# Kernel tuning notes

Measured on AMD Instinct MI355X. Metric: run time of the kernel, lower is better.

Reference implementation:

```python
import jax, jax.numpy as jnp
import numpy as np

D_MODEL = 768
NUM_HEADS = 8
DEPTH = D_MODEL // NUM_HEADS


def setup_inputs() -> dict:
    key = jax.random.key(0)
    ks = jax.random.split(key, 12)
    B, S = 4, 2048
    s = 0.02
    return {
        "q_in": jax.random.normal(ks[0], (B, S, D_MODEL), jnp.float32),
        "k_in": jax.random.normal(ks[1], (B, S, D_MODEL), jnp.float32),
        "v_in": jax.random.normal(ks[2], (B, S, D_MODEL), jnp.float32),
        "mask": jnp.zeros((B, 1, 1, S), jnp.float32),
        "wq": jax.random.normal(ks[3], (D_MODEL, D_MODEL), jnp.float32) * s,
        "bq": jax.random.normal(ks[4], (D_MODEL,), jnp.float32) * s,
        "wk": jax.random.normal(ks[5], (D_MODEL, D_MODEL), jnp.float32) * s,
        "bk": jax.random.normal(ks[6], (D_MODEL,), jnp.float32) * s,
        "wv": jax.random.normal(ks[7], (D_MODEL, D_MODEL), jnp.float32) * s,
        "bv": jax.random.normal(ks[8], (D_MODEL,), jnp.float32) * s,
        "wo": jax.random.normal(ks[9], (D_MODEL, D_MODEL), jnp.float32) * s,
        "bo": jax.random.normal(ks[10], (D_MODEL,), jnp.float32) * s,
    }


def _split_heads(x, B):
    # [B, S, D] -> [B, H, S, depth]
    return x.reshape(B, -1, NUM_HEADS, DEPTH).transpose(0, 2, 1, 3)


def reference(q_in, k_in, v_in, mask, wq, bq, wk, bk, wv, bv, wo, bo):
    B = q_in.shape[0]
    q = _split_heads(q_in @ wq + bq, B)   # [B,H,Sq,d]
    k = _split_heads(k_in @ wk + bk, B)   # [B,H,Sk,d]
    v = _split_heads(v_in @ wv + bv, B)   # [B,H,Sk,d]

    scale = 1.0 / jnp.sqrt(jnp.float32(DEPTH))
    logits = jnp.einsum("bhqd,bhkd->bhqk", q, k) * scale
    logits = logits + mask * (-1e9)
    attn = jax.nn.softmax(logits, axis=-1)            # [B,H,Sq,Sk]
    ctx = jnp.einsum("bhqk,bhkd->bhqd", attn, v)
    ctx = ctx.transpose(0, 2, 1, 3).reshape(B, -1, D_MODEL)  # concat heads
    out = ctx @ wo + bo
    return out, attn
```

## Files before the change

kernel.cpp:

```cpp
#include <hip/hip_runtime.h>
#include <hip/hip_bf16.h>
#include <stdint.h>


#define SEQ 2048
#define DM 768
#define NB 4
#define NH 8
#define DEP 96
#define MROWS 8192

typedef __bf16 bf16x8 __attribute__((ext_vector_type(8)));
typedef float f32x4 __attribute__((ext_vector_type(4)));

__device__ inline unsigned short f2b(float f) {
    return __builtin_bit_cast(unsigned short, (__bf16)f);
}
__device__ inline bf16x8 ld_frag(const unsigned short* p) {
    return __builtin_bit_cast(bf16x8, *(const uint4*)p);
}

__global__ __launch_bounds__(256) void wt_kernel(
    const float* __restrict__ w0, const float* __restrict__ w1,
    const float* __restrict__ w2, const float* __restrict__ w3,
    unsigned short* __restrict__ wt)
{
    __shared__ float tile[32][33];
    int mat = blockIdx.z;
    const float* w = mat == 0 ? w0 : mat == 1 ? w1 : mat == 2 ? w2 : w3;
    unsigned short* dst = wt + (size_t)mat * DM * DM;
    int k0 = blockIdx.x * 32, n0 = blockIdx.y * 32;
    int tx = threadIdx.x & 31, ty = threadIdx.x >> 5;
#pragma unroll
    for (int i = 0; i < 4; i++)
        tile[ty + i * 8][tx] = w[(size_t)(k0 + ty + i * 8) * DM + n0 + tx];
    __syncthreads();
#pragma unroll
    for (int i = 0; i < 4; i++)
        dst[(size_t)(n0 + ty + i * 8) * DM + k0 + tx] = f2b(tile[tx][ty + i * 8]);
}

__global__ __launch_bounds__(256) void proj_kernel(
    const float* __restrict__ qin, const float* __restrict__ kin, const float* __restrict__ vin,
    const unsigned short* __restrict__ wt,
    const float* __restrict__ bq, const float* __restrict__ bk, const float* __restrict__ bv,
    unsigned short* __restrict__ qb, unsigned short* __restrict__ kb, unsigned short* __restrict__ vb)
{
    int z = blockIdx.z;
    const float* x = z == 0 ? qin : z == 1 ? kin : vin;
    const unsigned short* W = wt + (size_t)z * DM * DM;
    const float* bias = z == 0 ? bq : z == 1 ? bk : bv;
    unsigned short* out = z == 0 ? qb : z == 1 ? kb : vb;

    int lane = threadIdx.x & 63, wv_ = threadIdx.x >> 6;
    int col = lane & 15, quad = lane >> 4;
    int m_base = blockIdx.x * 128 + (wv_ & 1) * 64;
    int n_base = blockIdx.y * 128 + (wv_ >> 1) * 64;

    f32x4 acc[4][4] = {};
    for (int kk = 0; kk < DM; kk += 32) {
        bf16x8 af[4], bfr[4];
#pragma unroll
        for (int mt = 0; mt < 4; mt++) {
            const float* src = x + (size_t)(m_base + mt * 16 + col) * DM + kk + quad * 8;
            float4 f0 = *(const float4*)src;
            float4 f1 = *(const float4*)(src + 4);
            bf16x8 a;
            a[0] = (__bf16)f0.x; a[1] = (__bf16)f0.y; a[2] = (__bf16)f0.z; a[3] = (__bf16)f0.w;
            a[4] = (__bf16)f1.x; a[5] = (__bf16)f1.y; a[6] = (__bf16)f1.z; a[7] = (__bf16)f1.w;
            af[mt] = a;
        }
#pragma unroll
        for (int nt = 0; nt < 4; nt++)
            bfr[nt] = ld_frag(W + (size_t)(n_base + nt * 16 + col) * DM + kk + quad * 8);
#pragma unroll
        for (int mt = 0; mt < 4; mt++)
#pragma unroll
            for (int nt = 0; nt < 4; nt++)
                acc[mt][nt] = __builtin_amdgcn_mfma_f32_16x16x32_bf16(af[mt], bfr[nt], acc[mt][nt], 0, 0, 0);
    }
#pragma unroll
    for (int mt = 0; mt < 4; mt++) {
        int grow_base = m_base + mt * 16 + quad * 4;
#pragma unroll
        for (int nt = 0; nt < 4; nt++) {
            int gcol = n_base + nt * 16 + col;
            float bv_ = bias[gcol];
            int h = gcol / DEP, d = gcol % DEP;
#pragma unroll
            for (int r = 0; r < 4; r++) {
                int grow = grow_base + r;
                int b = grow >> 11, s = grow & 2047;
                float v = acc[mt][nt][r] + bv_;
                out[((size_t)((b * NH + h) * SEQ + s)) * DEP + d] = f2b(v);
            }
        }
    }
}

__global__ __launch_bounds__(256) void vt_kernel(
    const unsigned short* __restrict__ vb, unsigned short* __restrict__ vt)
{
    __shared__ unsigned short tile[32][33];
    int bh = blockIdx.z;
    int s0 = blockIdx.x * 32, d0 = blockIdx.y * 32;
    int tx = threadIdx.x & 31, ty = threadIdx.x >> 5;
    const unsigned short* src = vb + (size_t)bh * SEQ * DEP;
    unsigned short* dst = vt + (size_t)bh * DEP * SEQ;
#pragma unroll
    for (int i = 0; i < 4; i++)
        tile[ty + i * 8][tx] = src[(size_t)(s0 + ty + i * 8) * DEP + d0 + tx];
    __syncthreads();
#pragma unroll
    for (int i = 0; i < 4; i++)
        dst[(size_t)(d0 + ty + i * 8) * SEQ + s0 + tx] = tile[tx][ty + i * 8];
}

__global__ __launch_bounds__(256) void attn_kernel(
    const unsigned short* __restrict__ qb, const unsigned short* __restrict__ kb,
    const unsigned short* __restrict__ vt, const float* __restrict__ mask,
    float* __restrict__ attn_out, unsigned short* __restrict__ ctx)
{
    __shared__ float mask_s[SEQ];
    __shared__ unsigned short k_lds[64 * 104];
    __shared__ unsigned short vt_lds[96 * 72];
    __shared__ unsigned short p_lds[4][16 * 72];

    int tid = threadIdx.x;
    int w = tid >> 6, lane = tid & 63, col = lane & 15, quad = lane >> 4;
    int bh = blockIdx.y;
    int b = bh >> 3, h = bh & 7;
    int q0 = blockIdx.x * 64 + w * 16;

    const unsigned short* Qp = qb + (size_t)bh * SEQ * DEP;
    const unsigned short* Kp = kb + (size_t)bh * SEQ * DEP;
    const unsigned short* Vp = vt + (size_t)bh * DEP * SEQ;
    float* attn = attn_out + (size_t)bh * SEQ * SEQ;

    for (int i = tid; i < SEQ; i += 256)
        mask_s[i] = mask[b * SEQ + i] * (-1e9f);

    bf16x8 aq[3];
#pragma unroll
    for (int ks = 0; ks < 3; ks++)
        aq[ks] = ld_frag(Qp + (size_t)(q0 + col) * DEP + ks * 32 + quad * 8);

    const float scale = 0.10206207261596575f;
    float lsum[4] = {0.f, 0.f, 0.f, 0.f};

    for (int kt = 0; kt < SEQ; kt += 64) {
        __syncthreads();
        for (int j = tid; j < 768; j += 256) {
            int row = j / 12, c = j % 12;
            *(uint4*)&k_lds[row * 104 + c * 8] = *(const uint4*)(Kp + (size_t)(kt + row) * DEP + c * 8);
        }
        __syncthreads();
#pragma unroll
        for (int nt = 0; nt < 4; nt++) {
            f32x4 c = {0.f, 0.f, 0.f, 0.f};
            int kr = nt * 16 + col;
#pragma unroll
            for (int ks = 0; ks < 3; ks++) {
                bf16x8 bk_ = ld_frag(&k_lds[kr * 104 + ks * 32 + quad * 8]);
                c = __builtin_amdgcn_mfma_f32_16x16x32_bf16(aq[ks], bk_, c, 0, 0, 0);
            }
            float mval = mask_s[kt + nt * 16 + col];
#pragma unroll
            for (int r = 0; r < 4; r++)
                lsum[r] += __expf(c[r] * scale + mval);
        }
    }
#pragma unroll
    for (int r = 0; r < 4; r++) {
        float v = lsum[r];
        v += __shfl_xor(v, 1); v += __shfl_xor(v, 2);
        v += __shfl_xor(v, 4); v += __shfl_xor(v, 8);
        lsum[r] = 1.0f / v;
    }

    f32x4 o[6] = {};
    for (int kt = 0; kt < SEQ; kt += 64) {
        __syncthreads();
        for (int j = tid; j < 768; j += 256) {
            int row = j / 12, c = j % 12;
            *(uint4*)&k_lds[row * 104 + c * 8] = *(const uint4*)(Kp + (size_t)(kt + row) * DEP + c * 8);
        }
        for (int j = tid; j < 768; j += 256) {
            int row = j >> 3, c = j & 7;
            *(uint4*)&vt_lds[row * 72 + c * 8] = *(const uint4*)(Vp + (size_t)row * SEQ + kt + c * 8);
        }
        __syncthreads();
#pragma unroll
        for (int nt = 0; nt < 4; nt++) {
            f32x4 c = {0.f, 0.f, 0.f, 0.f};
            int kr = nt * 16 + col;
#pragma unroll
            for (int ks = 0; ks < 3; ks++) {
                bf16x8 bk_ = ld_frag(&k_lds[kr * 104 + ks * 32 + quad * 8]);
                c = __builtin_amdgcn_mfma_f32_16x16x32_bf16(aq[ks], bk_, c, 0, 0, 0);
            }
            float mval = mask_s[kt + nt * 16 + col];
#pragma unroll
            for (int r = 0; r < 4; r++) {
                float p = __expf(c[r] * scale + mval) * lsum[r];
                attn[(size_t)(q0 + quad * 4 + r) * SEQ + kt + nt * 16 + col] = p;
                p_lds[w][(quad * 4 + r) * 72 + nt * 16 + col] = f2b(p);
            }
        }
        bf16x8 pa[2];
#pragma unroll
        for (int ks = 0; ks < 2; ks++)
            pa[ks] = ld_frag(&p_lds[w][col * 72 + ks * 32 + quad * 8]);
#pragma unroll
        for (int dt = 0; dt < 6; dt++) {
#pragma unroll
            for (int ks = 0; ks < 2; ks++) {
                bf16x8 bv_ = ld_frag(&vt_lds[(dt * 16 + col) * 72 + ks * 32 + quad * 8]);
                o[dt] = __builtin_amdgcn_mfma_f32_16x16x32_bf16(pa[ks], bv_, o[dt], 0, 0, 0);
            }
        }
    }
#pragma unroll
    for (int dt = 0; dt < 6; dt++)
#pragma unroll
        for (int r = 0; r < 4; r++) {
            int qrow = q0 + quad * 4 + r;
            ctx[(size_t)(b * SEQ + qrow) * DM + h * DEP + dt * 16 + col] = f2b(o[dt][r]);
        }
}

__global__ __launch_bounds__(256) void oproj_kernel(
    const unsigned short* __restrict__ ctx, const unsigned short* __restrict__ woT,
    const float* __restrict__ bo, float* __restrict__ out)
{
    int lane = threadIdx.x & 63, wv_ = threadIdx.x >> 6;
    int col = lane & 15, quad = lane >> 4;
    int m_base = blockIdx.x * 128 + (wv_ & 1) * 64;
    int n_base = blockIdx.y * 128 + (wv_ >> 1) * 64;

    f32x4 acc[4][4] = {};
    for (int kk = 0; kk < DM; kk += 32) {
        bf16x8 af[4], bfr[4];
#pragma unroll
        for (int mt = 0; mt < 4; mt++)
            af[mt] = ld_frag(ctx + (size_t)(m_base + mt * 16 + col) * DM + kk + quad * 8);
#pragma unroll
        for (int nt = 0; nt < 4; nt++)
            bfr[nt] = ld_frag(woT + (size_t)(n_base + nt * 16 + col) * DM + kk + quad * 8);
#pragma unroll
        for (int mt = 0; mt < 4; mt++)
#pragma unroll
            for (int nt = 0; nt < 4; nt++)
                acc[mt][nt] = __builtin_amdgcn_mfma_f32_16x16x32_bf16(af[mt], bfr[nt], acc[mt][nt], 0, 0, 0);
    }
#pragma unroll
    for (int mt = 0; mt < 4; mt++) {
        int grow_base = m_base + mt * 16 + quad * 4;
#pragma unroll
        for (int nt = 0; nt < 4; nt++) {
            int gcol = n_base + nt * 16 + col;
            float bv_ = bo[gcol];
#pragma unroll
            for (int r = 0; r < 4; r++)
                out[(size_t)(grow_base + r) * DM + gcol] = acc[mt][nt][r] + bv_;
        }
    }
}

extern "C" void kernel_launch(void* const* d_in, const int* in_sizes, int n_in,
                              void* d_out, int out_size, void* d_ws, size_t ws_size,
                              hipStream_t stream) {
    (void)in_sizes; (void)n_in; (void)out_size; (void)ws_size;
    const float* q_in = (const float*)d_in[0];
    const float* k_in = (const float*)d_in[1];
    const float* v_in = (const float*)d_in[2];
    const float* mask = (const float*)d_in[3];
    const float* wq = (const float*)d_in[4];
    const float* bq = (const float*)d_in[5];
    const float* wk = (const float*)d_in[6];
    const float* bk = (const float*)d_in[7];
    const float* wv = (const float*)d_in[8];
    const float* bv = (const float*)d_in[9];
    const float* wo = (const float*)d_in[10];
    const float* bo = (const float*)d_in[11];

    unsigned short* ws = (unsigned short*)d_ws;
    const size_t WMAT = (size_t)DM * DM;
    const size_t QKV = (size_t)NB * NH * SEQ * DEP;
    unsigned short* wT   = ws;
    unsigned short* qbuf = ws + 4 * WMAT;
    unsigned short* kbuf = qbuf + QKV;
    unsigned short* vbuf = kbuf + QKV;
    unsigned short* vtbuf = vbuf + QKV;
    unsigned short* ctxbuf = vtbuf + QKV;

    float* out_f = (float*)d_out;
    float* attn_f = out_f + (size_t)NB * SEQ * DM;

    dim3 blk(256);
    wt_kernel<<<dim3(24, 24, 4), blk, 0, stream>>>(wq, wk, wv, wo, wT);
    proj_kernel<<<dim3(MROWS / 128, DM / 128, 3), blk, 0, stream>>>(
        q_in, k_in, v_in, wT, bq, bk, bv, qbuf, kbuf, vbuf);
    vt_kernel<<<dim3(SEQ / 32, DEP / 32, NB * NH), blk, 0, stream>>>(vbuf, vtbuf);
    attn_kernel<<<dim3(SEQ / 64, NB * NH), blk, 0, stream>>>(
        qbuf, kbuf, vtbuf, mask, attn_f, ctxbuf);
    oproj_kernel<<<dim3(MROWS / 128, DM / 128), blk, 0, stream>>>(
        ctxbuf, wT + 3 * WMAT, bo, out_f);
}
```

Baseline: 1.131 ms.

## Stage GEMM tiles in LDS and read K/V directly from global in attention

The projection and output GEMMs now load each 128x32 A and B tile cooperatively into shared memory, with coalesced loads and one fp32-to-bf16 conversion per element, before issuing MFMAs from LDS. Previously each wave fetched its own fragments straight from global. The attention kernel drops its shared K and V^T staging and the associated barriers: each wave now reads K and V^T fragments directly from global through the cache, and launch bounds request 4 blocks per SM for higher occupancy. The risk is redundant global/L2 traffic in attention and extra barriers in the GEMMs.

```diff
diff --git a/kernel.cpp b/kernel.cpp
--- a/kernel.cpp
+++ b/kernel.cpp
@@ -46,33 +46,52 @@
     const float* __restrict__ bq, const float* __restrict__ bk, const float* __restrict__ bv,
     unsigned short* __restrict__ qb, unsigned short* __restrict__ kb, unsigned short* __restrict__ vb)
 {
+    __shared__ unsigned short As[128 * 32];
+    __shared__ unsigned short Bs[128 * 32];
+
     int z = blockIdx.z;
     const float* x = z == 0 ? qin : z == 1 ? kin : vin;
     const unsigned short* W = wt + (size_t)z * DM * DM;
     const float* bias = z == 0 ? bq : z == 1 ? bk : bv;
     unsigned short* out = z == 0 ? qb : z == 1 ? kb : vb;
 
-    int lane = threadIdx.x & 63, wv_ = threadIdx.x >> 6;
+    int tid = threadIdx.x;
+    int lane = tid & 63, wv_ = tid >> 6;
     int col = lane & 15, quad = lane >> 4;
-    int m_base = blockIdx.x * 128 + (wv_ & 1) * 64;
-    int n_base = blockIdx.y * 128 + (wv_ >> 1) * 64;
+    int m0 = blockIdx.x * 128, n0 = blockIdx.y * 128;
+    int mi = (wv_ & 1) * 64, ni = (wv_ >> 1) * 64;
+    int srow = tid >> 1, shalf = (tid & 1) * 16;
 
     f32x4 acc[4][4] = {};
     for (int kk = 0; kk < DM; kk += 32) {
+        __syncthreads();
+        {
+            const float* xa = x + (size_t)(m0 + srow) * DM + kk + shalf;
+            float4 f0 = *(const float4*)xa;
+            float4 f1 = *(const float4*)(xa + 4);
+            float4 f2 = *(const float4*)(xa + 8);
+            float4 f3 = *(const float4*)(xa + 12);
+            bf16x8 p0, p1;
+            p0[0] = (__bf16)f0.x; p0[1] = (__bf16)f0.y; p0[2] = (__bf16)f0.z; p0[3] = (__bf16)f0.w;
+            p0[4] = (__bf16)f1.x; p0[5] = (__bf16)f1.y; p0[6] = (__bf16)f1.z; p0[7] = (__bf16)f1.w;
+            p1[0] = (__bf16)f2.x; p1[1] = (__bf16)f2.y; p1[2] = (__bf16)f2.z; p1[3] = (__bf16)f2.w;
+            p1[4] = (__bf16)f3.x; p1[5] = (__bf16)f3.y; p1[6] = (__bf16)f3.z; p1[7] = (__bf16)f3.w;
+            *(uint4*)&As[srow * 32 + shalf]     = __builtin_bit_cast(uint4, p0);
+            *(uint4*)&As[srow * 32 + shalf + 8] = __builtin_bit_cast(uint4, p1);
+        }
+        {
+            const unsigned short* wb = W + (size_t)(n0 + srow) * DM + kk + shalf;
+            *(uint4*)&Bs[srow * 32 + shalf]     = *(const uint4*)wb;
+            *(uint4*)&Bs[srow * 32 + shalf + 8] = *(const uint4*)(wb + 8);
+        }
+        __syncthreads();
         bf16x8 af[4], bfr[4];
 #pragma unroll
-        for (int mt = 0; mt < 4; mt++) {
-            const float* src = x + (size_t)(m_base + mt * 16 + col) * DM + kk + quad * 8;
-            float4 f0 = *(const float4*)src;
-            float4 f1 = *(const float4*)(src + 4);
-            bf16x8 a;
-            a[0] = (__bf16)f0.x; a[1] = (__bf16)f0.y; a[2] = (__bf16)f0.z; a[3] = (__bf16)f0.w;
-            a[4] = (__bf16)f1.x; a[5] = (__bf16)f1.y; a[6] = (__bf16)f1.z; a[7] = (__bf16)f1.w;
-            af[mt] = a;
-        }
+        for (int mt = 0; mt < 4; mt++)
+            af[mt] = ld_frag(&As[(mi + mt * 16 + col) * 32 + quad * 8]);
 #pragma unroll
         for (int nt = 0; nt < 4; nt++)
-            bfr[nt] = ld_frag(W + (size_t)(n_base + nt * 16 + col) * DM + kk + quad * 8);
+            bfr[nt] = ld_frag(&Bs[(ni + nt * 16 + col) * 32 + quad * 8]);
 #pragma unroll
         for (int mt = 0; mt < 4; mt++)
 #pragma unroll
@@ -81,18 +100,17 @@
     }
 #pragma unroll
     for (int mt = 0; mt < 4; mt++) {
-        int grow_base = m_base + mt * 16 + quad * 4;
+        int grow_base = m0 + mi + mt * 16 + quad * 4;
 #pragma unroll
         for (int nt = 0; nt < 4; nt++) {
-            int gcol = n_base + nt * 16 + col;
+            int gcol = n0 + ni + nt * 16 + col;
             float bv_ = bias[gcol];
             int h = gcol / DEP, d = gcol % DEP;
 #pragma unroll
             for (int r = 0; r < 4; r++) {
                 int grow = grow_base + r;
                 int b = grow >> 11, s = grow & 2047;
-                float v = acc[mt][nt][r] + bv_;
-                out[((size_t)((b * NH + h) * SEQ + s)) * DEP + d] = f2b(v);
+                out[((size_t)((b * NH + h) * SEQ + s)) * DEP + d] = f2b(acc[mt][nt][r] + bv_);
             }
         }
     }
@@ -116,14 +134,12 @@
         dst[(size_t)(d0 + ty + i * 8) * SEQ + s0 + tx] = tile[tx][ty + i * 8];
 }
 
-__global__ __launch_bounds__(256) void attn_kernel(
+__global__ __launch_bounds__(256, 4) void attn_kernel(
     const unsigned short* __restrict__ qb, const unsigned short* __restrict__ kb,
     const unsigned short* __restrict__ vt, const float* __restrict__ mask,
     float* __restrict__ attn_out, unsigned short* __restrict__ ctx)
 {
     __shared__ float mask_s[SEQ];
-    __shared__ unsigned short k_lds[64 * 104];
-    __shared__ unsigned short vt_lds[96 * 72];
     __shared__ unsigned short p_lds[4][16 * 72];
 
     int tid = threadIdx.x;
@@ -139,6 +155,7 @@
 
     for (int i = tid; i < SEQ; i += 256)
         mask_s[i] = mask[b * SEQ + i] * (-1e9f);
+    __syncthreads();
 
     bf16x8 aq[3];
 #pragma unroll
@@ -149,25 +166,17 @@
     float lsum[4] = {0.f, 0.f, 0.f, 0.f};
 
     for (int kt = 0; kt < SEQ; kt += 64) {
-        __syncthreads();
-        for (int j = tid; j < 768; j += 256) {
-            int row = j / 12, c = j % 12;
-            *(uint4*)&k_lds[row * 104 + c * 8] = *(const uint4*)(Kp + (size_t)(kt + row) * DEP + c * 8);
-        }
-        __syncthreads();
 #pragma unroll
         for (int nt = 0; nt < 4; nt++) {
+            const unsigned short* kr = Kp + (size_t)(kt + nt * 16 + col) * DEP;
             f32x4 c = {0.f, 0.f, 0.f, 0.f};
-            int kr = nt * 16 + col;
-#pragma unroll
-            for (int ks = 0; ks < 3; ks++) {
-                bf16x8 bk_ = ld_frag(&k_lds[kr * 104 + ks * 32 + quad * 8]);
-                c = __builtin_amdgcn_mfma_f32_16x16x32_bf16(aq[ks], bk_, c, 0, 0, 0);
-            }
-            float mval = mask_s[kt + nt * 16 + col];
+#pragma unroll
+            for (int ks = 0; ks < 3; ks++)
+                c = __builtin_amdgcn_mfma_f32_16x16x32_bf16(aq[ks], ld_frag(kr + ks * 32 + quad * 8), c, 0, 0, 0);
+            float mv = mask_s[kt + nt * 16 + col];
 #pragma unroll
             for (int r = 0; r < 4; r++)
-                lsum[r] += __expf(c[r] * scale + mval);
+                lsum[r] += __expf(c[r] * scale + mv);
         }
     }
 #pragma unroll
@@ -180,44 +189,29 @@
 
     f32x4 o[6] = {};
     for (int kt = 0; kt < SEQ; kt += 64) {
-        __syncthreads();
-        for (int j = tid; j < 768; j += 256) {
-            int row = j / 12, c = j % 12;
-            *(uint4*)&k_lds[row * 104 + c * 8] = *(const uint4*)(Kp + (size_t)(kt + row) * DEP + c * 8);
-        }
-        for (int j = tid; j < 768; j += 256) {
-            int row = j >> 3, c = j & 7;
-            *(uint4*)&vt_lds[row * 72 + c * 8] = *(const uint4*)(Vp + (size_t)row * SEQ + kt + c * 8);
-        }
-        __syncthreads();
 #pragma unroll
         for (int nt = 0; nt < 4; nt++) {
+            const unsigned short* kr = Kp + (size_t)(kt + nt * 16 + col) * DEP;
             f32x4 c = {0.f, 0.f, 0.f, 0.f};
-            int kr = nt * 16 + col;
-#pragma unroll
-            for (int ks = 0; ks < 3; ks++) {
-                bf16x8 bk_ = ld_frag(&k_lds[kr * 104 + ks * 32 + quad * 8]);
-                c = __builtin_amdgcn_mfma_f32_16x16x32_bf16(aq[ks], bk_, c, 0, 0, 0);
-            }
-            float mval = mask_s[kt + nt * 16 + col];
+#pragma unroll
+            for (int ks = 0; ks < 3; ks++)
+                c = __builtin_amdgcn_mfma_f32_16x16x32_bf16(aq[ks], ld_frag(kr + ks * 32 + quad * 8), c, 0, 0, 0);
+            float mv = mask_s[kt + nt * 16 + col];
 #pragma unroll
             for (int r = 0; r < 4; r++) {
-                float p = __expf(c[r] * scale + mval) * lsum[r];
+                float p = __expf(c[r] * scale + mv) * lsum[r];
                 attn[(size_t)(q0 + quad * 4 + r) * SEQ + kt + nt * 16 + col] = p;
                 p_lds[w][(quad * 4 + r) * 72 + nt * 16 + col] = f2b(p);
             }
         }
-        bf16x8 pa[2];
-#pragma unroll
-        for (int ks = 0; ks < 2; ks++)
-            pa[ks] = ld_frag(&p_lds[w][col * 72 + ks * 32 + quad * 8]);
+        bf16x8 pa0 = ld_frag(&p_lds[w][col * 72 + quad * 8]);
+        bf16x8 pa1 = ld_frag(&p_lds[w][col * 72 + 32 + quad * 8]);
+        const unsigned short* vbase = Vp + (size_t)col * SEQ + kt;
 #pragma unroll
         for (int dt = 0; dt < 6; dt++) {
-#pragma unroll
-            for (int ks = 0; ks < 2; ks++) {
-                bf16x8 bv_ = ld_frag(&vt_lds[(dt * 16 + col) * 72 + ks * 32 + quad * 8]);
-                o[dt] = __builtin_amdgcn_mfma_f32_16x16x32_bf16(pa[ks], bv_, o[dt], 0, 0, 0);
-            }
+            const unsigned short* vr = vbase + (size_t)dt * 16 * SEQ;
+            o[dt] = __builtin_amdgcn_mfma_f32_16x16x32_bf16(pa0, ld_frag(vr + quad * 8), o[dt], 0, 0, 0);
+            o[dt] = __builtin_amdgcn_mfma_f32_16x16x32_bf16(pa1, ld_frag(vr + 32 + quad * 8), o[dt], 0, 0, 0);
         }
     }
 #pragma unroll
@@ -233,20 +227,35 @@
     const unsigned short* __restrict__ ctx, const unsigned short* __restrict__ woT,
     const float* __restrict__ bo, float* __restrict__ out)
 {
-    int lane = threadIdx.x & 63, wv_ = threadIdx.x >> 6;
+    __shared__ unsigned short As[128 * 32];
+    __shared__ unsigned short Bs[128 * 32];
+
+    int tid = threadIdx.x;
+    int lane = tid & 63, wv_ = tid >> 6;
     int col = lane & 15, quad = lane >> 4;
-    int m_base = blockIdx.x * 128 + (wv_ & 1) * 64;
-    int n_base = blockIdx.y * 128 + (wv_ >> 1) * 64;
+    int m0 = blockIdx.x * 128, n0 = blockIdx.y * 128;
+    int mi = (wv_ & 1) * 64, ni = (wv_ >> 1) * 64;
+    int srow = tid >> 1, shalf = (tid & 1) * 16;
 
     f32x4 acc[4][4] = {};
     for (int kk = 0; kk < DM; kk += 32) {
+        __syncthreads();
+        {
+            const unsigned short* xa = ctx + (size_t)(m0 + srow) * DM + kk + shalf;
+            *(uint4*)&As[srow * 32 + shalf]     = *(const uint4*)xa;
+            *(uint4*)&As[srow * 32 + shalf + 8] = *(const uint4*)(xa + 8);
+            const unsigned short* wb = woT + (size_t)(n0 + srow) * DM + kk + shalf;
+            *(uint4*)&Bs[srow * 32 + shalf]     = *(const uint4*)wb;
+            *(uint4*)&Bs[srow * 32 + shalf + 8] = *(const uint4*)(wb + 8);
+        }
+        __syncthreads();
         bf16x8 af[4], bfr[4];
 #pragma unroll
         for (int mt = 0; mt < 4; mt++)
-            af[mt] = ld_frag(ctx + (size_t)(m_base + mt * 16 + col) * DM + kk + quad * 8);
+            af[mt] = ld_frag(&As[(mi + mt * 16 + col) * 32 + quad * 8]);
 #pragma unroll
         for (int nt = 0; nt < 4; nt++)
-            bfr[nt] = ld_frag(woT + (size_t)(n_base + nt * 16 + col) * DM + kk + quad * 8);
+            bfr[nt] = ld_frag(&Bs[(ni + nt * 16 + col) * 32 + quad * 8]);
 #pragma unroll
         for (int mt = 0; mt < 4; mt++)
 #pragma unroll
@@ -255,10 +264,10 @@
     }
 #pragma unroll
     for (int mt = 0; mt < 4; mt++) {
-        int grow_base = m_base + mt * 16 + quad * 4;
+        int grow_base = m0 + mi + mt * 16 + quad * 4;
 #pragma unroll
         for (int nt = 0; nt < 4; nt++) {
-            int gcol = n_base + nt * 16 + col;
+            int gcol = n0 + ni + nt * 16 + col;
             float bv_ = bo[gcol];
 #pragma unroll
             for (int r = 0; r < 4; r++)
@@ -287,10 +296,10 @@
     unsigned short* ws = (unsigned short*)d_ws;
     const size_t WMAT = (size_t)DM * DM;
     const size_t QKV = (size_t)NB * NH * SEQ * DEP;
-    unsigned short* wT   = ws;
-    unsigned short* qbuf = ws + 4 * WMAT;
-    unsigned short* kbuf = qbuf + QKV;
-    unsigned short* vbuf = kbuf + QKV;
+    unsigned short* wT    = ws;
+    unsigned short* qbuf  = ws + 4 * WMAT;
+    unsigned short* kbuf  = qbuf + QKV;
+    unsigned short* vbuf  = kbuf + QKV;
     unsigned short* vtbuf = vbuf + QKV;
     unsigned short* ctxbuf = vtbuf + QKV;
 
```

Result: faster. 1.085 ms (-4.1%).
